# Optimization experiments

Measured on AMD Instinct MI355X. Metric: run time of the kernel, lower is better.

Reference implementation:

```python
import jax, jax.numpy as jnp
import numpy as np

B, H, C = 131072, 16, 32        # batch, n_holidays, n_changepoints
HID, HP, SKU = 512, 512 // 16, 64  # hidden_dim, hidden per holiday, sku embed dim
TEMP = 0.7
TIME_MAX = 365.0
LN_EPS = 1e-3  # keras LayerNormalization default epsilon


def mish(x):
    return x * jnp.tanh(jax.nn.softplus(x))


def setup_inputs() -> dict:
    key = jax.random.key(0)
    ks = jax.random.split(key, 12)
    inputs = jax.random.uniform(ks[0], (B, H), dtype=jnp.float32) * TIME_MAX
    sku_embedding = jax.random.normal(ks[1], (B, SKU), dtype=jnp.float32)
    # per-holiday params, stacked over holiday axis
    deltas = jnp.full((H, C), TIME_MAX / C, dtype=jnp.float32)  # changepoint_deltas init
    ln_gamma = jnp.ones((H, C), dtype=jnp.float32)
    ln_beta = jnp.zeros((H, C), dtype=jnp.float32)
    attn_w = jax.random.normal(ks[2], (H,), dtype=jnp.float32) * 0.5  # Dense(1) on [...,1]
    Wh = jax.random.normal(ks[3], (H, C, HP), dtype=jnp.float32) * (1.0 / np.sqrt(C))
    Wah = jax.random.normal(ks[4], (HID, HID), dtype=jnp.float32) * (1.0 / np.sqrt(HID))
    Waa = jax.random.normal(ks[5], (HID, HID), dtype=jnp.float32) * (1.0 / np.sqrt(HID))
    Wb = jax.random.normal(ks[6], (SKU, HID), dtype=jnp.float32) * (1.0 / np.sqrt(SKU))
    Wa = jax.random.normal(ks[7], (SKU, HID), dtype=jnp.float32) * (1.0 / np.sqrt(SKU))
    Wo = jax.random.normal(ks[8], (HID, 1), dtype=jnp.float32)
    Wo = Wo / jnp.linalg.norm(Wo, axis=0, keepdims=True)  # UnitNorm(axis=0) constraint
    return {"inputs": inputs, "sku_embedding": sku_embedding, "deltas": deltas,
            "ln_gamma": ln_gamma, "ln_beta": ln_beta, "attn_w": attn_w, "Wh": Wh,
            "Wah": Wah, "Waa": Waa, "Wb": Wb, "Wa": Wa, "Wo": Wo}


def reference(inputs, sku_embedding, deltas, ln_gamma, ln_beta, attn_w, Wh, Wah, Waa, Wb, Wa, Wo):
    # ChangepointReLU (vectorised over holidays): softplus -> cumsum -> rescale to [0, 365]
    pd = jax.nn.softplus(deltas)                     # [H, C]
    cps = jnp.cumsum(pd, axis=-1)
    cps = cps / cps[:, -1:] * TIME_MAX               # time_min = 0
    feats = jax.nn.relu(inputs[:, :, None] - cps[None, :, :])  # [B, H, C]
    # per-holiday LayerNorm over changepoint axis
    mu = jnp.mean(feats, axis=-1, keepdims=True)
    var = jnp.mean((feats - mu) ** 2, axis=-1, keepdims=True)
    normed = (feats - mu) * jax.lax.rsqrt(var + LN_EPS) * ln_gamma[None] + ln_beta[None]
    # per-holiday attention: Dense(1,no bias) on [...,1] == scalar multiply per holiday
    logits = normed * attn_w[None, :, None]
    attn = jax.nn.softmax(logits / TEMP, axis=-1)    # n_changepoints > 1
    attended = normed * attn                          # [B, H, C]
    # per-holiday hidden Dense(HP, mish, no bias), then concat over holidays
    hid = mish(jnp.einsum('bhc,hcd->bhd', attended, Wh))  # [B, H, HP]
    aggregated = hid.reshape(hid.shape[0], H * HP)        # [B, HID]
    agg_hidden = mish(aggregated @ Wah)                   # [B, HID]
    agg_attn = jax.nn.softmax((agg_hidden @ Waa) / TEMP, axis=-1)
    final = agg_hidden * agg_attn                         # dropout inactive (inference)
    beta = jax.nn.sigmoid(sku_embedding @ Wb)
    alpha = sku_embedding @ Wa
    final = final * beta + alpha
    return final @ Wo                                     # [B, 1]
```

## Files before the change

kernel.cpp:

```cpp
#include <hip/hip_runtime.h>
#include <hip/hip_fp16.h>
#include <stdint.h>

#define B_TOT 131072
#define CHUNK 65536
#define NH 16
#define NC 32
#define HIDD 512

typedef unsigned short u16;
typedef unsigned int u32;
typedef __attribute__((ext_vector_type(8))) short short8;
typedef __attribute__((ext_vector_type(4))) float f32x4;
typedef __attribute__((ext_vector_type(4))) int i32x4;

#define GLLDS(g, l) __builtin_amdgcn_global_load_lds((const __attribute__((address_space(1))) unsigned int*)(g), (__attribute__((address_space(3))) unsigned int*)(l), 16, 0, 0)

__device__ __forceinline__ u16 f2bf(float x){
  unsigned u = __float_as_uint(x);
  u += 0x7fffu + ((u >> 16) & 1u);
  return (u16)(u >> 16);
}
__device__ __forceinline__ float bf2f(u16 b){ return __uint_as_float(((unsigned)b) << 16); }
__device__ __forceinline__ u16 f2h(float x){ __half h = __float2half(x); return *(u16*)&h; }
__device__ __forceinline__ float h2f(u16 b){ __half h; *(u16*)&h = b; return __half2float(h); }
__device__ __forceinline__ float mishf(float x){
  float e = __expf(fminf(x, 30.f));
  float u = 1.f + e;
  float u2 = u * u;
  return x * (u2 - 1.f) / (u2 + 1.f);
}

__global__ void prep_small(const float* __restrict__ deltas, const float* __restrict__ Wa,
                           const float* __restrict__ Wo, float* __restrict__ cps, float* __restrict__ wWo)
{
  const int t = threadIdx.x;
  if (t < NH){
    float cum[NC];
    float run = 0.f;
#pragma unroll
    for (int c = 0; c < NC; c++){
      float d = deltas[t*NC + c];
      float sp = (d > 20.f) ? d : log1pf(__expf(d));
      run += sp; cum[c] = run;
    }
    float s = 365.0f / run;
#pragma unroll
    for (int c = 0; c < NC; c++) cps[t*NC + c] = cum[c] * s;
  } else if (t >= 64 && t < 128){
    const int k = t - 64;
    float s = 0.f;
    for (int n = 0; n < HIDD; n++) s += Wa[k*HIDD + n] * Wo[n];
    wWo[k] = s;
  }
}

__global__ void prep_convert(const float* __restrict__ Wah, const float* __restrict__ Waa,
                             const float* __restrict__ Wb, const float* __restrict__ Wh,
                             u16* __restrict__ WahT, u16* __restrict__ WaaT,
                             u16* __restrict__ WbT, u16* __restrict__ WhT)
{
  int i = blockIdx.x * 256 + threadIdx.x;
  if (i < 262144){ int n = i >> 9, k = i & 511; WahT[i] = f2bf(Wah[k*512 + n]); return; }
  i -= 262144;
  if (i < 262144){ int n = i >> 9, k = i & 511; WaaT[i] = f2bf(Waa[k*512 + n]); return; }
  i -= 262144;
  if (i < 32768){ int n = i >> 6, k = i & 63; WbT[i] = f2bf(Wb[k*512 + n]); return; }
  i -= 32768;
  if (i < 16384){ int h = i >> 10, r = i & 1023, d = r >> 5, c = r & 31;
                  WhT[i] = f2bf(Wh[h*1024 + c*32 + d]); return; }
}

__global__ __launch_bounds__(256) void stage1_kernel(
    const float* __restrict__ inputs, const float* __restrict__ sku,
    const float* __restrict__ ln_g, const float* __restrict__ ln_b,
    const float* __restrict__ attnw, const float* __restrict__ cps,
    const float* __restrict__ wWo, const u16* __restrict__ WhT,
    u16* __restrict__ agg, u16* __restrict__ skub, float* __restrict__ skd)
{
  __shared__ __align__(16) float in_l[256];
  __shared__ __align__(16) float cps_l[512];
  __shared__ __align__(16) float gam_l[512];
  __shared__ __align__(16) float bet_l[512];
  __shared__ float aw_l[16];
  __shared__ __align__(16) u16 at_l[16*16*32];
  __shared__ __align__(16) u16 ot_l[16*512];

  const int t = threadIdx.x;
  const int ln = t & 63;
  const long bb = (long)blockIdx.x * 16;

  in_l[t] = inputs[bb*16 + t];
  cps_l[t] = cps[t];       cps_l[t+256] = cps[t+256];
  gam_l[t] = ln_g[t];      gam_l[t+256] = ln_g[t+256];
  bet_l[t] = ln_b[t];      bet_l[t+256] = ln_b[t+256];
  if (t < 16) aw_l[t] = attnw[t];
  {
    const f32x4 sv = *(const f32x4*)&sku[bb*64 + t*4];
    unsigned lo = (unsigned)f2bf(sv.x) | ((unsigned)f2bf(sv.y) << 16);
    unsigned hi = (unsigned)f2bf(sv.z) | ((unsigned)f2bf(sv.w) << 16);
    unsigned long long v = (unsigned long long)lo | ((unsigned long long)hi << 32);
    *(unsigned long long*)&skub[bb*64 + t*4] = v;
    const f32x4 wv4 = *(const f32x4*)&wWo[(ln & 15)*4];
    float pd = sv.x*wv4.x + sv.y*wv4.y + sv.z*wv4.z + sv.w*wv4.w;
#pragma unroll
    for (int s = 1; s < 16; s <<= 1) pd += __shfl_xor(pd, s);
    if ((ln & 15) == 0) skd[bb + (t >> 4)] = pd;
  }
  __syncthreads();

  const int h = t >> 4, bi = t & 15;
  const float x = in_l[bi*16 + h];
  float nrm[NC];
  float s1 = 0.f;
#pragma unroll
  for (int c = 0; c < NC; c++){ float f = fmaxf(x - cps_l[h*NC + c], 0.f); nrm[c] = f; s1 += f; }
  const float mu = s1 * (1.f/NC);
  float s2 = 0.f;
#pragma unroll
  for (int c = 0; c < NC; c++){ float d = nrm[c] - mu; s2 += d*d; }
  const float rs = rsqrtf(s2 * (1.f/NC) + 1e-3f);
  const float aw = aw_l[h] * (1.0f/0.7f);
  float lmax = -1e30f;
#pragma unroll
  for (int c = 0; c < NC; c++){
    float nv = (nrm[c] - mu) * rs * gam_l[h*NC + c] + bet_l[h*NC + c];
    nrm[c] = nv;
    lmax = fmaxf(lmax, nv * aw);
  }
  float ps = 0.f;
#pragma unroll
  for (int c = 0; c < NC; c++) ps += __expf(nrm[c]*aw - lmax);
  const float invs = 1.f / ps;
#pragma unroll
  for (int c = 0; c < NC; c += 2){
    const float p0 = __expf(nrm[c]*aw - lmax) * invs;
    const float p1 = __expf(nrm[c+1]*aw - lmax) * invs;
    unsigned pk = (unsigned)f2bf(nrm[c]*p0) | ((unsigned)f2bf(nrm[c+1]*p1) << 16);
    *(unsigned*)&at_l[h*512 + bi*32 + c] = pk;
  }
  __syncthreads();

  const int wv = t >> 6;
  const int lrow = ln & 15, lq = ln >> 4;
#pragma unroll
  for (int q = 0; q < 4; q++){
    const int hh = wv*4 + q;
    short8 af  = *(const short8*)&at_l[hh*512 + lrow*32 + lq*8];
    short8 bf0 = *(const short8*)&WhT[hh*1024 + lrow*32 + lq*8];
    short8 bf1 = *(const short8*)&WhT[hh*1024 + (16 + lrow)*32 + lq*8];
    f32x4 acc0 = {0.f,0.f,0.f,0.f}, acc1 = {0.f,0.f,0.f,0.f};
    acc0 = __builtin_amdgcn_mfma_f32_16x16x32_bf16(af, bf0, acc0, 0, 0, 0);
    acc1 = __builtin_amdgcn_mfma_f32_16x16x32_bf16(af, bf1, acc1, 0, 0, 0);
#pragma unroll
    for (int r = 0; r < 4; r++){
      const int br = lq*4 + r;
      ot_l[br*512 + hh*32 + lrow]      = f2bf(mishf(acc0[r]));
      ot_l[br*512 + hh*32 + 16 + lrow] = f2bf(mishf(acc1[r]));
    }
  }
  __syncthreads();
  {
    const int row = t >> 4, c16 = t & 15;
    const i32x4* src = (const i32x4*)&ot_l[row*512 + c16*32];
    i32x4* dst = (i32x4*)&agg[(bb + row)*512 + c16*32];
#pragma unroll
    for (int j = 0; j < 4; j++) dst[j] = src[j];
  }
}

__global__ __launch_bounds__(256, 3) void gemm1(
    const u16* __restrict__ A, const u16* __restrict__ Bt, u16* __restrict__ aggh)
{
  __shared__ __align__(16) u16 smem[24576];
  const int t = threadIdx.x, wv = t >> 6, ln = t & 63;
  const int g = blockIdx.x;
  const int m_idx = (g & 7) + ((g >> 5) << 3);
  const int n_idx = (g >> 3) & 3;
  const long m0 = (long)m_idx * 128;
  const int n0 = n_idx * 128;
  const int lrow = ln & 15, lq = ln >> 4;
  const int wm = wv >> 1, wn = wv & 1;

  auto stage = [&](int buf, int kt){
#pragma unroll
    for (int p = 0; p < 2; p++){
      const int chunk = p*256 + wv*64 + ln;
      const int mm = chunk >> 2, kc = chunk & 3;
      const int kcl = kc ^ ((mm >> 1) & 3);
      GLLDS(&A[(m0 + mm)*512 + kt + kcl*8],  &smem[buf*4096 + (p*256 + wv*64)*8]);
      GLLDS(&Bt[(n0 + mm)*512 + kt + kcl*8], &smem[12288 + buf*4096 + (p*256 + wv*64)*8]);
    }
  };

  f32x4 acc[4][4] = {};
  stage(0, 0); stage(1, 32);
#pragma unroll 1
  for (int ks = 0; ks < 16; ks++){
    const int cur = ks % 3;
    if (ks < 15) asm volatile("s_waitcnt vmcnt(4)" ::: "memory");
    else         asm volatile("s_waitcnt vmcnt(0)" ::: "memory");
    __builtin_amdgcn_s_barrier();
    if (ks + 2 < 16) stage((ks + 2) % 3, (ks + 2)*32);
    short8 a[4], b[4];
#pragma unroll
    for (int i = 0; i < 4; i++){
      const int ra = wm*64 + i*16 + lrow;
      const int rb = wn*64 + i*16 + lrow;
      const int lqa = lq ^ ((ra >> 1) & 3);
      const int lqb = lq ^ ((rb >> 1) & 3);
      a[i] = *(const short8*)&smem[cur*4096 + ra*32 + lqa*8];
      b[i] = *(const short8*)&smem[12288 + cur*4096 + rb*32 + lqb*8];
    }
#pragma unroll
    for (int i = 0; i < 4; i++)
#pragma unroll
      for (int j = 0; j < 4; j++)
        acc[i][j] = __builtin_amdgcn_mfma_f32_16x16x32_bf16(a[i], b[j], acc[i][j], 0, 0, 0);
  }

  const int TP = 136;
  __syncthreads();
#pragma unroll 1
  for (int h = 0; h < 2; h++){
    if (wm == h){
#pragma unroll
      for (int i = 0; i < 4; i++)
#pragma unroll
        for (int j = 0; j < 4; j++)
#pragma unroll
          for (int r = 0; r < 4; r++)
            smem[(i*16 + lq*4 + r)*TP + wn*64 + j*16 + lrow] = f2bf(mishf(acc[i][j][r]));
    }
    __syncthreads();
#pragma unroll
    for (int it = 0; it < 4; it++){
      const int idx = it*256 + t;
      const int row = idx >> 4, ch = idx & 15;
      const i32x4 v = *(const i32x4*)&smem[row*TP + ch*8];
      *(i32x4*)&aggh[(m0 + h*64 + row)*512 + n0 + ch*8] = v;
    }
    __syncthreads();
  }
}

__global__ __launch_bounds__(256, 3) void mega2f(
    const u16* __restrict__ A, const u16* __restrict__ Bt,
    const u16* __restrict__ skub, const u16* __restrict__ WbT,
    const float* __restrict__ Wo, float* __restrict__ part)
{
  __shared__ __align__(16) u16 smem[24576];
  const int t = threadIdx.x, wv = t >> 6, ln = t & 63;
  const int g = blockIdx.x;
  const int m_idx = (g & 7) + ((g >> 5) << 3);
  const int n_idx = (g >> 3) & 3;
  const long m0 = (long)m_idx * 128;
  const int n0 = n_idx * 128;
  const int lrow = ln & 15, lq = ln >> 4;
  const int wm = wv >> 1, wn = wv & 1;
  const float inv_t = 1.0f / 0.7f;

  u32 bwp[4][4][2];
  {
    auto stage3 = [&](int buf, int kt){
#pragma unroll
      for (int p = 0; p < 2; p++){
        const int chunk = p*256 + wv*64 + ln;
        const int mm = chunk >> 2, kc = chunk & 3;
        const int kcl = kc ^ ((mm >> 1) & 3);
        GLLDS(&skub[(m0 + mm)*64 + kt + kcl*8], &smem[buf*4096 + (p*256 + wv*64)*8]);
        GLLDS(&WbT[(n0 + mm)*64 + kt + kcl*8],  &smem[8192 + buf*4096 + (p*256 + wv*64)*8]);
      }
    };
    f32x4 acc3[4][4] = {};
    stage3(0, 0); stage3(1, 32);
    asm volatile("s_waitcnt vmcnt(0)" ::: "memory");
    __builtin_amdgcn_s_barrier();
#pragma unroll
    for (int ks3 = 0; ks3 < 2; ks3++){
      short8 a3[4], b3[4];
#pragma unroll
      for (int i = 0; i < 4; i++){
        const int ra = wm*64 + i*16 + lrow;
        const int rb = wn*64 + i*16 + lrow;
        const int lqa = lq ^ ((ra >> 1) & 3);
        const int lqb = lq ^ ((rb >> 1) & 3);
        a3[i] = *(const short8*)&smem[ks3*4096 + ra*32 + lqa*8];
        b3[i] = *(const short8*)&smem[8192 + ks3*4096 + rb*32 + lqb*8];
      }
#pragma unroll
      for (int i = 0; i < 4; i++)
#pragma unroll
        for (int j = 0; j < 4; j++)
          acc3[i][j] = __builtin_amdgcn_mfma_f32_16x16x32_bf16(a3[i], b3[j], acc3[i][j], 0, 0, 0);
    }
#pragma unroll
    for (int j = 0; j < 4; j++){
      const float wo = Wo[n0 + wn*64 + j*16 + lrow];
#pragma unroll
      for (int i = 0; i < 4; i++)
#pragma unroll
        for (int rp = 0; rp < 2; rp++){
          const float s0 = wo / (1.f + __expf(-acc3[i][j][2*rp]));
          const float s1 = wo / (1.f + __expf(-acc3[i][j][2*rp+1]));
          bwp[i][j][rp] = (u32)f2h(s0) | ((u32)f2h(s1) << 16);
        }
    }
  }
  __syncthreads();

  auto stage = [&](int buf, int kt){
#pragma unroll
    for (int p = 0; p < 2; p++){
      const int chunk = p*256 + wv*64 + ln;
      const int mm = chunk >> 2, kc = chunk & 3;
      const int kcl = kc ^ ((mm >> 1) & 3);
      GLLDS(&A[(m0 + mm)*512 + kt + kcl*8],  &smem[buf*4096 + (p*256 + wv*64)*8]);
      GLLDS(&Bt[(n0 + mm)*512 + kt + kcl*8], &smem[12288 + buf*4096 + (p*256 + wv*64)*8]);
    }
  };

  f32x4 acc[4][4] = {};
  stage(0, 0); stage(1, 32);
#pragma unroll 1
  for (int ks = 0; ks < 16; ks++){
    const int cur = ks % 3;
    if (ks < 15) asm volatile("s_waitcnt vmcnt(4)" ::: "memory");
    else         asm volatile("s_waitcnt vmcnt(0)" ::: "memory");
    __builtin_amdgcn_s_barrier();
    if (ks + 2 < 16) stage((ks + 2) % 3, (ks + 2)*32);
    short8 a[4], b[4];
#pragma unroll
    for (int i = 0; i < 4; i++){
      const int ra = wm*64 + i*16 + lrow;
      const int rb = wn*64 + i*16 + lrow;
      const int lqa = lq ^ ((ra >> 1) & 3);
      const int lqb = lq ^ ((rb >> 1) & 3);
      a[i] = *(const short8*)&smem[cur*4096 + ra*32 + lqa*8];
      b[i] = *(const short8*)&smem[12288 + cur*4096 + rb*32 + lqb*8];
    }
#pragma unroll
    for (int i = 0; i < 4; i++)
#pragma unroll
      for (int j = 0; j < 4; j++)
        acc[i][j] = __builtin_amdgcn_mfma_f32_16x16x32_bf16(a[i], b[j], acc[i][j], 0, 0, 0);
  }

  __syncthreads();
#pragma unroll
  for (int it = 0; it < 8; it++){
    const int idx = it*256 + wv*64 + ln;
    const int row = idx >> 4, gcol = idx & 15;
    GLLDS(&A[(m0 + row)*512 + n0 + ((gcol ^ (row & 7)) << 3)], &smem[(it*256 + wv*64)*8]);
  }
  asm volatile("s_waitcnt vmcnt(0)" ::: "memory");
  __syncthreads();

  float* mloc = (float*)&smem[16384];
  float* sloc = mloc + 256;
  float* tloc = sloc + 256;

#pragma unroll
  for (int i = 0; i < 4; i++){
#pragma unroll
    for (int r = 0; r < 4; r++){
      float tm = acc[i][0][r];
#pragma unroll
      for (int j = 1; j < 4; j++) tm = fmaxf(tm, acc[i][j][r]);
#pragma unroll
      for (int s = 1; s < 16; s <<= 1) tm = fmaxf(tm, __shfl_xor(tm, s));
      const int rowL = wm*64 + i*16 + lq*4 + r;
      float sp = 0.f, tp = 0.f;
#pragma unroll
      for (int j = 0; j < 4; j++){
        const int colL = wn*64 + j*16 + lrow;
        const float e = __expf((acc[i][j][r] - tm) * inv_t);
        const float av = bf2f(smem[rowL*128 + (((colL >> 3) ^ (rowL & 7)) << 3) + (colL & 7)]);
        const u16 bh = (u16)(bwp[i][j][r >> 1] >> ((r & 1)*16));
        sp += e; tp += e * av * h2f(bh);
      }
#pragma unroll
      for (int s = 1; s < 16; s <<= 1){ sp += __shfl_xor(sp, s); tp += __shfl_xor(tp, s); }
      if (lrow == 0){
        mloc[rowL*2 + wn] = tm; sloc[rowL*2 + wn] = sp; tloc[rowL*2 + wn] = tp;
      }
    }
  }
  __syncthreads();
  if (t < 128){
    const float ma = mloc[t*2], mb = mloc[t*2 + 1];
    const float M = fmaxf(ma, mb);
    const float wa = __expf((ma - M) * inv_t), wb = __expf((mb - M) * inv_t);
    const float S = sloc[t*2]*wa + sloc[t*2 + 1]*wb;
    const float T = tloc[t*2]*wa + tloc[t*2 + 1]*wb;
    float* pm = part + (size_t)n_idx*3*CHUNK;
    pm[m0 + t]           = M;
    pm[CHUNK + m0 + t]   = S;
    pm[2*CHUNK + m0 + t] = T;
  }
}

__global__ __launch_bounds__(256) void combine_kernel(
    const float* __restrict__ part, const float* __restrict__ skd, float* __restrict__ outp)
{
  const int row = blockIdx.x*256 + threadIdx.x;
  const float inv_t = 1.0f / 0.7f;
  float M = -1e30f;
#pragma unroll
  for (int nt = 0; nt < 4; nt++) M = fmaxf(M, part[(size_t)nt*3*CHUNK + row]);
  float S = 0.f, T = 0.f;
#pragma unroll
  for (int nt = 0; nt < 4; nt++){
    const float w = __expf((part[(size_t)nt*3*CHUNK + row] - M) * inv_t);
    S += part[(size_t)nt*3*CHUNK + CHUNK + row] * w;
    T += part[(size_t)nt*3*CHUNK + 2*CHUNK + row] * w;
  }
  outp[row] = T / S + skd[row];
}

__global__ void ws_too_small(float* o, float v){ o[(long)blockIdx.x*256 + threadIdx.x] = v; }

extern "C" void kernel_launch(void* const* d_in, const int* in_sizes, int n_in,
                              void* d_out, int out_size, void* d_ws, size_t ws_size,
                              hipStream_t stream)
{
  const float* inputs = (const float*)d_in[0];
  const float* sku    = (const float*)d_in[1];
  const float* deltas = (const float*)d_in[2];
  const float* ln_g   = (const float*)d_in[3];
  const float* ln_b   = (const float*)d_in[4];
  const float* attnw  = (const float*)d_in[5];
  const float* Wh     = (const float*)d_in[6];
  const float* Wah    = (const float*)d_in[7];
  const float* Waa    = (const float*)d_in[8];
  const float* Wb     = (const float*)d_in[9];
  const float* Wa     = (const float*)d_in[10];
  const float* Wo     = (const float*)d_in[11];
  float* outp = (float*)d_out;

  const size_t OFF_CPS  = 0;
  const size_t OFF_WWO  = 2048;
  const size_t OFF_WAHT = 4096;
  const size_t OFF_WAAT = OFF_WAHT + 524288;
  const size_t OFF_WBT  = OFF_WAAT + 524288;
  const size_t OFF_WHT  = OFF_WBT  + 65536;
  const size_t OFF_SKUB = OFF_WHT  + 32768;
  const size_t OFF_SKD  = OFF_SKUB + (size_t)CHUNK*64*2;
  const size_t OFF_AGG  = OFF_SKD  + (size_t)CHUNK*4;
  const size_t OFF_AGH  = OFF_AGG  + (size_t)CHUNK*512*2;
  const size_t OFF_PART = OFF_AGH  + (size_t)CHUNK*512*2;
  const size_t NEED     = OFF_PART + (size_t)4*3*CHUNK*4;

  if (ws_size < NEED){
    hipLaunchKernelGGL(ws_too_small, dim3(B_TOT/256), dim3(256), 0, stream,
                       outp, -(float)(ws_size >> 20));
    return;
  }

  char* ws = (char*)d_ws;
  float* cps  = (float*)(ws + OFF_CPS);
  float* wWo  = (float*)(ws + OFF_WWO);
  u16* WahT   = (u16*)(ws + OFF_WAHT);
  u16* WaaT   = (u16*)(ws + OFF_WAAT);
  u16* WbT    = (u16*)(ws + OFF_WBT);
  u16* WhT    = (u16*)(ws + OFF_WHT);
  u16* skub   = (u16*)(ws + OFF_SKUB);
  float* skd  = (float*)(ws + OFF_SKD);
  u16* agg    = (u16*)(ws + OFF_AGG);
  u16* aggh   = (u16*)(ws + OFF_AGH);
  float* part = (float*)(ws + OFF_PART);

  hipLaunchKernelGGL(prep_small, dim3(1), dim3(128), 0, stream, deltas, Wa, Wo, cps, wWo);
  hipLaunchKernelGGL(prep_convert, dim3(2240), dim3(256), 0, stream,
                     Wah, Waa, Wb, Wh, WahT, WaaT, WbT, WhT);

  for (int ch = 0; ch < B_TOT / CHUNK; ch++){
    const float* in_c  = inputs + (size_t)ch * CHUNK * 16;
    const float* sku_c = sku    + (size_t)ch * CHUNK * 64;
    float* out_c       = outp   + (size_t)ch * CHUNK;

    hipLaunchKernelGGL(stage1_kernel, dim3(CHUNK/16), dim3(256), 0, stream,
                       in_c, sku_c, ln_g, ln_b, attnw, cps, wWo, WhT, agg, skub, skd);
    hipLaunchKernelGGL(gemm1, dim3(CHUNK/128*4), dim3(256), 0, stream,
                       agg, WahT, aggh);
    hipLaunchKernelGGL(mega2f, dim3(CHUNK/128*4), dim3(256), 0, stream,
                       aggh, WaaT, skub, WbT, Wo, part);
    hipLaunchKernelGGL(combine_kernel, dim3(CHUNK/256), dim3(256), 0, stream,
                       part, skd, out_c);
  }
}
```

Before: 485.4 us.

## Process four row tiles per stage1 block and use fast reciprocals

Each stage1 block now handles 64 batch rows in four sequential 16-row iterations. The Wh MFMA fragments are loaded into registers once and the per-block LayerNorm/gamma/beta/cps shared loads are amortised across the iterations. The next tile's inputs are prefetched after the first barrier. Divisions in mish, the softmax normaliser and the sigmoid epilogue are replaced with hardware approximate reciprocals. The trade-offs are fewer blocks in the grid, extra barriers per iteration, more register pressure from the held fragments, and slightly lower reciprocal precision.

```diff
diff --git a/kernel.cpp b/kernel.cpp
--- a/kernel.cpp
+++ b/kernel.cpp
@@ -28,7 +28,7 @@
   float e = __expf(fminf(x, 30.f));
   float u = 1.f + e;
   float u2 = u * u;
-  return x * (u2 - 1.f) / (u2 + 1.f);
+  return x * (u2 - 1.f) * __builtin_amdgcn_rcpf(u2 + 1.f);
 }
 
 __global__ void prep_small(const float* __restrict__ deltas, const float* __restrict__ Wa,
@@ -88,84 +88,102 @@
 
   const int t = threadIdx.x;
   const int ln = t & 63;
-  const long bb = (long)blockIdx.x * 16;
-
-  in_l[t] = inputs[bb*16 + t];
+  const long bb = (long)blockIdx.x * 64;
+
   cps_l[t] = cps[t];       cps_l[t+256] = cps[t+256];
   gam_l[t] = ln_g[t];      gam_l[t+256] = ln_g[t+256];
   bet_l[t] = ln_b[t];      bet_l[t+256] = ln_b[t+256];
   if (t < 16) aw_l[t] = attnw[t];
-  {
-    const f32x4 sv = *(const f32x4*)&sku[bb*64 + t*4];
+  in_l[t] = inputs[bb*16 + t];
+
+#pragma unroll
+  for (int it = 0; it < 4; it++){
+    const long bs = bb + it*16;
+    const f32x4 sv = *(const f32x4*)&sku[bs*64 + t*4];
     unsigned lo = (unsigned)f2bf(sv.x) | ((unsigned)f2bf(sv.y) << 16);
     unsigned hi = (unsigned)f2bf(sv.z) | ((unsigned)f2bf(sv.w) << 16);
     unsigned long long v = (unsigned long long)lo | ((unsigned long long)hi << 32);
-    *(unsigned long long*)&skub[bb*64 + t*4] = v;
+    *(unsigned long long*)&skub[bs*64 + t*4] = v;
     const f32x4 wv4 = *(const f32x4*)&wWo[(ln & 15)*4];
     float pd = sv.x*wv4.x + sv.y*wv4.y + sv.z*wv4.z + sv.w*wv4.w;
 #pragma unroll
     for (int s = 1; s < 16; s <<= 1) pd += __shfl_xor(pd, s);
-    if ((ln & 15) == 0) skd[bb + (t >> 4)] = pd;
-  }
-  __syncthreads();
+    if ((ln & 15) == 0) skd[bs + (t >> 4)] = pd;
+  }
 
   const int h = t >> 4, bi = t & 15;
-  const float x = in_l[bi*16 + h];
-  float nrm[NC];
-  float s1 = 0.f;
-#pragma unroll
-  for (int c = 0; c < NC; c++){ float f = fmaxf(x - cps_l[h*NC + c], 0.f); nrm[c] = f; s1 += f; }
-  const float mu = s1 * (1.f/NC);
-  float s2 = 0.f;
-#pragma unroll
-  for (int c = 0; c < NC; c++){ float d = nrm[c] - mu; s2 += d*d; }
-  const float rs = rsqrtf(s2 * (1.f/NC) + 1e-3f);
-  const float aw = aw_l[h] * (1.0f/0.7f);
-  float lmax = -1e30f;
-#pragma unroll
-  for (int c = 0; c < NC; c++){
-    float nv = (nrm[c] - mu) * rs * gam_l[h*NC + c] + bet_l[h*NC + c];
-    nrm[c] = nv;
-    lmax = fmaxf(lmax, nv * aw);
-  }
-  float ps = 0.f;
-#pragma unroll
-  for (int c = 0; c < NC; c++) ps += __expf(nrm[c]*aw - lmax);
-  const float invs = 1.f / ps;
-#pragma unroll
-  for (int c = 0; c < NC; c += 2){
-    const float p0 = __expf(nrm[c]*aw - lmax) * invs;
-    const float p1 = __expf(nrm[c+1]*aw - lmax) * invs;
-    unsigned pk = (unsigned)f2bf(nrm[c]*p0) | ((unsigned)f2bf(nrm[c+1]*p1) << 16);
-    *(unsigned*)&at_l[h*512 + bi*32 + c] = pk;
-  }
-  __syncthreads();
-
   const int wv = t >> 6;
   const int lrow = ln & 15, lq = ln >> 4;
+  const float aw = aw_l[h] * (1.0f/0.7f);
+
+  short8 wf0[4], wf1[4];
 #pragma unroll
   for (int q = 0; q < 4; q++){
     const int hh = wv*4 + q;
-    short8 af  = *(const short8*)&at_l[hh*512 + lrow*32 + lq*8];
-    short8 bf0 = *(const short8*)&WhT[hh*1024 + lrow*32 + lq*8];
-    short8 bf1 = *(const short8*)&WhT[hh*1024 + (16 + lrow)*32 + lq*8];
-    f32x4 acc0 = {0.f,0.f,0.f,0.f}, acc1 = {0.f,0.f,0.f,0.f};
-    acc0 = __builtin_amdgcn_mfma_f32_16x16x32_bf16(af, bf0, acc0, 0, 0, 0);
-    acc1 = __builtin_amdgcn_mfma_f32_16x16x32_bf16(af, bf1, acc1, 0, 0, 0);
-#pragma unroll
-    for (int r = 0; r < 4; r++){
-      const int br = lq*4 + r;
-      ot_l[br*512 + hh*32 + lrow]      = f2bf(mishf(acc0[r]));
-      ot_l[br*512 + hh*32 + 16 + lrow] = f2bf(mishf(acc1[r]));
-    }
+    wf0[q] = *(const short8*)&WhT[hh*1024 + lrow*32 + lq*8];
+    wf1[q] = *(const short8*)&WhT[hh*1024 + (16 + lrow)*32 + lq*8];
   }
   __syncthreads();
-  {
-    const int row = t >> 4, c16 = t & 15;
-    const i32x4* src = (const i32x4*)&ot_l[row*512 + c16*32];
-    i32x4* dst = (i32x4*)&agg[(bb + row)*512 + c16*32];
-#pragma unroll
-    for (int j = 0; j < 4; j++) dst[j] = src[j];
+
+#pragma unroll 1
+  for (int it = 0; it < 4; it++){
+    const float x = in_l[bi*16 + h];
+    const float awv = aw_l[h] * (1.0f/0.7f);
+    float nrm[NC];
+    float s1 = 0.f;
+#pragma unroll
+    for (int c = 0; c < NC; c++){ float f = fmaxf(x - cps_l[h*NC + c], 0.f); nrm[c] = f; s1 += f; }
+    const float mu = s1 * (1.f/NC);
+    float s2 = 0.f;
+#pragma unroll
+    for (int c = 0; c < NC; c++){ float d = nrm[c] - mu; s2 += d*d; }
+    const float rs = rsqrtf(s2 * (1.f/NC) + 1e-3f);
+    float lmax = -1e30f;
+#pragma unroll
+    for (int c = 0; c < NC; c++){
+      float nv = (nrm[c] - mu) * rs * gam_l[h*NC + c] + bet_l[h*NC + c];
+      nrm[c] = nv;
+      lmax = fmaxf(lmax, nv * awv);
+    }
+    float ps = 0.f;
+#pragma unroll
+    for (int c = 0; c < NC; c++) ps += __expf(nrm[c]*awv - lmax);
+    const float invs = __builtin_amdgcn_rcpf(ps);
+#pragma unroll
+    for (int c = 0; c < NC; c += 2){
+      const float p0 = __expf(nrm[c]*awv - lmax) * invs;
+      const float p1 = __expf(nrm[c+1]*awv - lmax) * invs;
+      unsigned pk = (unsigned)f2bf(nrm[c]*p0) | ((unsigned)f2bf(nrm[c+1]*p1) << 16);
+      *(unsigned*)&at_l[h*512 + bi*32 + c] = pk;
+    }
+    __syncthreads();
+
+    if (it < 3) in_l[t] = inputs[(bb + (it+1)*16)*16 + t];
+
+#pragma unroll
+    for (int q = 0; q < 4; q++){
+      const int hh = wv*4 + q;
+      short8 af = *(const short8*)&at_l[hh*512 + lrow*32 + lq*8];
+      f32x4 acc0 = {0.f,0.f,0.f,0.f}, acc1 = {0.f,0.f,0.f,0.f};
+      acc0 = __builtin_amdgcn_mfma_f32_16x16x32_bf16(af, wf0[q], acc0, 0, 0, 0);
+      acc1 = __builtin_amdgcn_mfma_f32_16x16x32_bf16(af, wf1[q], acc1, 0, 0, 0);
+#pragma unroll
+      for (int r = 0; r < 4; r++){
+        const int br = lq*4 + r;
+        ot_l[br*512 + hh*32 + lrow]      = f2bf(mishf(acc0[r]));
+        ot_l[br*512 + hh*32 + 16 + lrow] = f2bf(mishf(acc1[r]));
+      }
+    }
+    __syncthreads();
+
+    {
+      const int row = t >> 4, c16 = t & 15;
+      const i32x4* src = (const i32x4*)&ot_l[row*512 + c16*32];
+      i32x4* dst = (i32x4*)&agg[(bb + it*16 + row)*512 + c16*32];
+#pragma unroll
+      for (int j = 0; j < 4; j++) dst[j] = src[j];
+    }
+    __syncthreads();
   }
 }
 
@@ -301,8 +319,8 @@
       for (int i = 0; i < 4; i++)
 #pragma unroll
         for (int rp = 0; rp < 2; rp++){
-          const float s0 = wo / (1.f + __expf(-acc3[i][j][2*rp]));
-          const float s1 = wo / (1.f + __expf(-acc3[i][j][2*rp+1]));
+          const float s0 = wo * __builtin_amdgcn_rcpf(1.f + __expf(-acc3[i][j][2*rp]));
+          const float s1 = wo * __builtin_amdgcn_rcpf(1.f + __expf(-acc3[i][j][2*rp+1]));
           bwp[i][j][rp] = (u32)f2h(s0) | ((u32)f2h(s1) << 16);
         }
     }
@@ -479,7 +497,7 @@
     const float* sku_c = sku    + (size_t)ch * CHUNK * 64;
     float* out_c       = outp   + (size_t)ch * CHUNK;
 
-    hipLaunchKernelGGL(stage1_kernel, dim3(CHUNK/16), dim3(256), 0, stream,
+    hipLaunchKernelGGL(stage1_kernel, dim3(CHUNK/64), dim3(256), 0, stream,
                        in_c, sku_c, ln_g, ln_b, attnw, cps, wWo, WhT, agg, skub, skd);
     hipLaunchKernelGGL(gemm1, dim3(CHUNK/128*4), dim3(256), 0, stream,
                        agg, WahT, aggh);
```

Measured after the change: 454.6 us. -6.4%, faster.
